# Kernel tuning notes

Measured on AMD Instinct MI355X. Metric: run time of the kernel, lower is better.

The kernel has to match this reference:

```python
import jax, jax.numpy as jnp
import numpy as np

G = 512       # field_size
SIGMA = 0.5   # causal kernel decay
H = 16        # num_heads


def _kernel_fft():
    # causal exponential kernel: k[i] = exp(-(center-i)/sigma) for i<=center else 0
    i = jnp.arange(G, dtype=jnp.float32)
    center = G // 2
    k = jnp.where(i <= center, jnp.exp(-(center - i) / SIGMA), 0.0)
    k = k / (k.sum() + 1e-8)
    return jnp.fft.rfft(k)  # [G//2+1] complex


def setup_inputs() -> dict:
    key = jax.random.key(0)
    ks = jax.random.split(key, 5)
    B, N, D = 4, 8192, 1024
    s = 1.0 / np.sqrt(D)
    return {
        "x": jax.random.normal(ks[0], (B, N, D), jnp.float32),
        "Wqkv": jax.random.normal(ks[1], (3 * D, D), jnp.float32) * s,
        "bqkv": jax.random.normal(ks[2], (3 * D,), jnp.float32) * 0.01,
        "Wout": jax.random.normal(ks[3], (D, D), jnp.float32) * s,
        "bout": jax.random.normal(ks[4], (D,), jnp.float32) * 0.01,
    }


def reference(x, Wqkv, bqkv, Wout, bout):
    B, N, D = x.shape
    hd = D // H
    qkv = x @ Wqkv.T + bqkv                       # [B,N,3D]
    q, k, v = jnp.split(qkv, 3, axis=-1)          # q is computed but unused (as in source)
    k = k.reshape(B, N, H, hd).transpose(0, 2, 1, 3)   # [B,H,N,hd]
    v = v.reshape(B, N, H, hd).transpose(0, 2, 1, 3)
    # map sequence positions to field bins
    seq_pos = jnp.arange(N, dtype=jnp.float32)
    field_idx = jnp.clip((seq_pos / max(N - 1, 1) * (G - 1)).astype(jnp.int32), 0, G - 1)  # [N]
    # deposit = v * |k|, scattered into the field buffer
    k_mag = jnp.linalg.norm(k, axis=-1, keepdims=True)  # [B,H,N,1]
    deposit = v * k_mag                                  # [B,H,N,hd]
    field = jnp.zeros((B, H, G, hd), x.dtype).at[:, :, field_idx, :].add(deposit)
    # causal (circular) convolution via FFT along field axis
    kf = _kernel_fft()
    field = jnp.fft.irfft(jnp.fft.rfft(field, axis=2) * kf[None, None, :, None], n=G, axis=2)
    # gather back at each token's bin
    out = field[:, :, field_idx, :]                      # [B,H,N,hd]
    out = out.transpose(0, 2, 1, 3).reshape(B, N, D)
    return out @ Wout.T + bout
```

## Files before the change

kernel.cpp:

```cpp
#include <hip/hip_runtime.h>

#define BB 4
#define NN 8192
#define DD 1024
#define HH 16
#define HD 64
#define GG 512

typedef short short8 __attribute__((ext_vector_type(8)));
typedef float f32x4 __attribute__((ext_vector_type(4)));

__device__ __forceinline__ unsigned short f2bf(float f) {
  union { float f; unsigned int u; } v; v.f = f;
  unsigned int r = v.u + 0x7FFFu + ((v.u >> 16) & 1u);
  return (unsigned short)(r >> 16);
}
__device__ __forceinline__ float bf2f(unsigned short b) {
  union { unsigned int u; float f; } v; v.u = ((unsigned int)b) << 16;
  return v.f;
}

__device__ __forceinline__ void gload16(const void* g, void* l) {
  __builtin_amdgcn_global_load_lds((const __attribute__((address_space(1))) void*)g,
                                   (__attribute__((address_space(3))) void*)l,
                                   16, 0, 0);
}

__global__ void cvt_all(const float* __restrict__ x, const float* __restrict__ Wqkv,
                        const float* __restrict__ Wout,
                        unsigned short* __restrict__ xb, unsigned short* __restrict__ wkb,
                        unsigned short* __restrict__ wvb, unsigned short* __restrict__ woutb) {
  const int total = 8388608 + 3 * 262144;
  int stride = gridDim.x * blockDim.x;
  for (int j = blockIdx.x * blockDim.x + threadIdx.x; j < total; j += stride) {
    const float4* s; ushort4* d; int r;
    if (j < 8388608) { s = (const float4*)x; d = (ushort4*)xb; r = j; }
    else {
      int q = j - 8388608; int seg = q >> 18; r = q & 262143;
      if (seg == 0)      { s = (const float4*)(Wqkv + 1048576); d = (ushort4*)wkb; }
      else if (seg == 1) { s = (const float4*)(Wqkv + 2097152); d = (ushort4*)wvb; }
      else               { s = (const float4*)Wout;             d = (ushort4*)woutb; }
    }
    float4 f = s[r];
    ushort4 u;
    u.x = f2bf(f.x); u.y = f2bf(f.y); u.z = f2bf(f.z); u.w = f2bf(f.w);
    d[r] = u;
  }
}

__global__ __launch_bounds__(256) void xw_kernel(
    const unsigned short* __restrict__ xb, const float* __restrict__ kw,
    unsigned short* __restrict__ xwb, float* __restrict__ sw) {
  __shared__ float w_l[20][16];
  __shared__ int mflag[20];
  const int bg = blockIdx.x;
  const int b = bg >> 9, g = bg & 511;
  const int t = threadIdx.x;
  int lo = (g * (NN - 1)) / (GG - 1) - 2;
  if (lo < 0) lo = 0;
  if (t < 20) {
    int n = lo + t;
    mflag[t] = (n < NN) && ((int)(((float)n / 8191.0f) * 511.0f) == g);
  }
  for (int u = t; u < 320; u += 256) {
    int ln = u >> 4, h = u & 15;
    int n = lo + ln;
    float w = 0.0f;
    if (n < NN && (int)(((float)n / 8191.0f) * 511.0f) == g)
      w = kw[((size_t)(b * NN + n)) * 16 + h];
    w_l[ln][h] = w;
  }
  __syncthreads();
  if (t < 16) {
    float s = 0.0f;
    #pragma unroll
    for (int ln = 0; ln < 20; ++ln) s += w_l[ln][t];
    sw[bg * 16 + t] = s;
  }
  float acc[16][4] = {};
  const int c0 = t * 4;
  for (int ln = 0; ln < 20; ++ln) {
    if (!mflag[ln]) continue;
    int n = lo + ln;
    ushort4 xv = *(const ushort4*)(xb + ((size_t)(b * NN + n)) * 1024 + c0);
    float x0 = bf2f(xv.x), x1 = bf2f(xv.y), x2 = bf2f(xv.z), x3 = bf2f(xv.w);
    #pragma unroll
    for (int h = 0; h < 16; ++h) {
      float w = w_l[ln][h];
      acc[h][0] += w * x0; acc[h][1] += w * x1;
      acc[h][2] += w * x2; acc[h][3] += w * x3;
    }
  }
  #pragma unroll
  for (int h = 0; h < 16; ++h) {
    ushort4 o;
    o.x = f2bf(acc[h][0]); o.y = f2bf(acc[h][1]);
    o.z = f2bf(acc[h][2]); o.w = f2bf(acc[h][3]);
    *(ushort4*)(xwb + ((size_t)h * 2048 + bg) * 1024 + c0) = o;
  }
}

__global__ __launch_bounds__(256, 2) void field_gemm(
    const unsigned short* __restrict__ xwb, const unsigned short* __restrict__ wvb,
    const float* __restrict__ sw, const float* __restrict__ bv,
    float* __restrict__ field2) {
  __shared__ __align__(16) unsigned short As[2][64 * 32];
  __shared__ __align__(16) unsigned short Bs[2][64 * 32];
  const int h = blockIdx.x >> 5;
  const int mb = blockIdx.x & 31;
  const int t = threadIdx.x;
  const int wv_ = t >> 6, lane = t & 63;
  const int l15 = lane & 15, sr = lane >> 4;

  const unsigned short* Ah = xwb + (size_t)h * 2048 * 1024 + (size_t)mb * 64 * 1024;
  const unsigned short* Bh = wvb + (size_t)h * 64 * 1024;

  const int srow = wv_ * 16 + (lane >> 2);
  const int sg = (lane & 3) ^ ((srow >> 1) & 3);
  const int dL = wv_ * 1024;

  const unsigned short* aG = Ah + (size_t)srow * 1024 + sg * 8;
  const unsigned short* bG = Bh + (size_t)srow * 1024 + sg * 8;

  auto stage = [&](int tt, int q) {
    gload16(aG + tt * 32, (char*)As[q] + dL);
    gload16(bG + tt * 32, (char*)Bs[q] + dL);
  };

  int aOff, bOff[4];
  {
    int r = wv_ * 16 + l15;
    aOff = r * 64 + ((sr ^ ((r >> 1) & 3)) * 16);
  }
  #pragma unroll
  for (int j = 0; j < 4; ++j) {
    int r = j * 16 + l15;
    bOff[j] = r * 64 + ((sr ^ ((r >> 1) & 3)) * 16);
  }

  f32x4 acc[4] = {};
  stage(0, 0);
  for (int tt = 0; tt < 32; ++tt) {
    if (tt + 1 < 32) {
      stage(tt + 1, (tt + 1) & 1);
      asm volatile("s_waitcnt vmcnt(2)" ::: "memory");
    } else {
      asm volatile("s_waitcnt vmcnt(0)" ::: "memory");
    }
    __builtin_amdgcn_s_barrier();
    const char* a = (const char*)As[tt & 1];
    const char* bb = (const char*)Bs[tt & 1];
    short8 aF = *(const short8*)(a + aOff);
    short8 bF[4];
    #pragma unroll
    for (int j = 0; j < 4; ++j) bF[j] = *(const short8*)(bb + bOff[j]);
    #pragma unroll
    for (int j = 0; j < 4; ++j)
      acc[j] = __builtin_amdgcn_mfma_f32_16x16x32_bf16(aF, bF[j], acc[j], 0, 0, 0);
    __builtin_amdgcn_s_barrier();
  }

  const int row0 = mb * 64 + wv_ * 16 + sr * 4;
  #pragma unroll
  for (int r = 0; r < 4; ++r) {
    float swv = sw[(row0 + r) * 16 + h];
    #pragma unroll
    for (int j = 0; j < 4; ++j) {
      int col = h * 64 + j * 16 + l15;
      field2[(size_t)(row0 + r) * 1024 + col] = acc[j][r] + swv * bv[col];
    }
  }
}

__global__ __launch_bounds__(256, 4) void gemm64(
    const unsigned short* __restrict__ A, const unsigned short* __restrict__ Bm,
    const float* __restrict__ bias, float* __restrict__ C,
    int M, int N, int K) {
  __shared__ __align__(16) unsigned short As[2][64 * 32];
  __shared__ __align__(16) unsigned short Bs[2][64 * 32];
  const int nb = N >> 6;
  const int mb = blockIdx.x / nb, nk = blockIdx.x % nb;
  const int t = threadIdx.x;
  const int wv_ = t >> 6, lane = t & 63;
  const int l15 = lane & 15, sr = lane >> 4;
  const int nt = K >> 5;

  const unsigned short* Ab = A + (size_t)mb * 64 * K;
  const unsigned short* Bb = Bm + (size_t)nk * 64 * K;

  const int srow = wv_ * 16 + (lane >> 2);
  const int sg = (lane & 3) ^ ((srow >> 1) & 3);
  const int dL = wv_ * 1024;

  const unsigned short* aG = Ab + (size_t)srow * K + sg * 8;
  const unsigned short* bG = Bb + (size_t)srow * K + sg * 8;

  auto stage = [&](int tt, int q) {
    gload16(aG + tt * 32, (char*)As[q] + dL);
    gload16(bG + tt * 32, (char*)Bs[q] + dL);
  };

  int aOff, bOff[4];
  {
    int r = wv_ * 16 + l15;
    aOff = r * 64 + ((sr ^ ((r >> 1) & 3)) * 16);
  }
  #pragma unroll
  for (int j = 0; j < 4; ++j) {
    int r = j * 16 + l15;
    bOff[j] = r * 64 + ((sr ^ ((r >> 1) & 3)) * 16);
  }

  f32x4 acc[4] = {};
  stage(0, 0);
  for (int tt = 0; tt < nt; ++tt) {
    if (tt + 1 < nt) {
      stage(tt + 1, (tt + 1) & 1);
      asm volatile("s_waitcnt vmcnt(2)" ::: "memory");
    } else {
      asm volatile("s_waitcnt vmcnt(0)" ::: "memory");
    }
    __builtin_amdgcn_s_barrier();
    const char* a = (const char*)As[tt & 1];
    const char* bb = (const char*)Bs[tt & 1];
    short8 aF = *(const short8*)(a + aOff);
    short8 bF[4];
    #pragma unroll
    for (int j = 0; j < 4; ++j) bF[j] = *(const short8*)(bb + bOff[j]);
    #pragma unroll
    for (int j = 0; j < 4; ++j)
      acc[j] = __builtin_amdgcn_mfma_f32_16x16x32_bf16(aF, bF[j], acc[j], 0, 0, 0);
    __builtin_amdgcn_s_barrier();
  }

  const int row0 = mb * 64 + wv_ * 16 + sr * 4;
  #pragma unroll
  for (int r = 0; r < 4; ++r) {
    #pragma unroll
    for (int j = 0; j < 4; ++j) {
      int col = nk * 64 + j * 16 + l15;
      C[(size_t)(row0 + r) * N + col] = acc[j][r] + bias[col];
    }
  }
}

__global__ void conv_kernel(const float* __restrict__ field2,
                            unsigned short* __restrict__ fconv2) {
  int i = blockIdx.x * blockDim.x + threadIdx.x;
  int c4 = i & 255;
  int bg = i >> 8;
  int b = bg >> 9, g = bg & 511;
  const float4* f4 = (const float4*)field2;
  float w = 0.86466471f;
  const float dec = 0.13533528f;
  float4 s = {0.f, 0.f, 0.f, 0.f};
  #pragma unroll
  for (int m = 0; m <= 20; ++m) {
    float4 v = f4[(size_t)((b << 9) + ((g + 256 + m) & 511)) * 256 + c4];
    s.x += w * v.x; s.y += w * v.y; s.z += w * v.z; s.w += w * v.w;
    w *= dec;
  }
  ushort4 o;
  o.x = f2bf(s.x); o.y = f2bf(s.y); o.z = f2bf(s.z); o.w = f2bf(s.w);
  *(ushort4*)(fconv2 + (size_t)bg * 1024 + c4 * 4) = o;
}

__global__ void expand_kernel(const float* __restrict__ small,
                              float* __restrict__ out) {
  const int total = 32768 * 256;
  int stride = gridDim.x * blockDim.x;
  for (int i = blockIdx.x * blockDim.x + threadIdx.x; i < total; i += stride) {
    int m = i >> 8;
    int b = m >> 13, n = m & (NN - 1);
    int g = (int)(((float)n / 8191.0f) * 511.0f);
    ((float4*)out)[i] = ((const float4*)small)[(((b << 9) + g) << 8) + (i & 255)];
  }
}

__global__ __launch_bounds__(512, 2) void gemm_knorm(
    const unsigned short* __restrict__ A, const unsigned short* __restrict__ Bm,
    const float* __restrict__ bias, float* __restrict__ Cout,
    int M, int N, int K) {
  __shared__ __align__(16) unsigned short smem[4 * 16384];

  const int t512 = threadIdx.x;
  const int wv = t512 >> 6, lane = t512 & 63;
  const int wm = wv >> 2, wn = wv & 3;
  const int l15 = lane & 15, sr = lane >> 4;
  const int nt = K >> 5;

  const int nwg = gridDim.x;
  const int lin = blockIdx.x;
  const int swz = (lin & 7) * (nwg >> 3) + (lin >> 3);
  const int gx = N >> 8;
  const int bm = (swz / gx) * 256;
  const int bn = (swz % gx) * 256;

  const int srow0 = wv * 16 + (lane >> 2);
  const int sg = (lane & 3) ^ ((srow0 >> 1) & 3);
  const int aL0 = wv * 1024;
  const int aL1 = 8192 + wv * 1024;

  const unsigned short* aG0 = A + (size_t)(bm + srow0) * K + sg * 8;
  const unsigned short* aG1 = A + (size_t)(bm + srow0 + 128) * K + sg * 8;
  const unsigned short* bG0 = Bm + (size_t)(bn + srow0) * K + sg * 8;
  const unsigned short* bG1 = Bm + (size_t)(bn + srow0 + 128) * K + sg * 8;

  auto stageA = [&](int t, int q) {
    char* base = (char*)smem + q * 32768;
    gload16(aG0 + (size_t)t * 32, base + aL0);
    gload16(aG1 + (size_t)t * 32, base + aL1);
  };
  auto stageB = [&](int t, int q) {
    char* base = (char*)smem + q * 32768;
    gload16(bG0 + (size_t)t * 32, base + 16384 + aL0);
    gload16(bG1 + (size_t)t * 32, base + 16384 + aL1);
  };

  int aOffB[8], bOffB[4];
  #pragma unroll
  for (int i = 0; i < 8; ++i) {
    int r = wm * 128 + i * 16 + l15;
    aOffB[i] = r * 64 + ((sr ^ ((r >> 1) & 3)) * 16);
  }
  #pragma unroll
  for (int j = 0; j < 4; ++j) {
    int r = wn * 64 + j * 16 + l15;
    bOffB[j] = r * 64 + ((sr ^ ((r >> 1) & 3)) * 16);
  }

  f32x4 acc[8][4] = {};

  stageA(0, 0); stageB(0, 0);
  stageA(1, 1); stageB(1, 1);
  stageA(2, 2); stageB(2, 2);
  asm volatile("s_waitcnt vmcnt(8)" ::: "memory");
  __builtin_amdgcn_s_barrier();

  for (int t = 0; t < nt; ++t) {
    const char* base = (const char*)smem + (t & 3) * 32768;
    short8 aF[8], bF[4];

    if (t + 3 < nt) stageA(t + 3, (t + 3) & 3);
    #pragma unroll
    for (int i = 0; i < 4; ++i) aF[i] = *(const short8*)(base + aOffB[i]);
    #pragma unroll
    for (int j = 0; j < 4; ++j) bF[j] = *(const short8*)(base + 16384 + bOffB[j]);
    __builtin_amdgcn_s_barrier();
    __builtin_amdgcn_s_setprio(1);
    #pragma unroll
    for (int i = 0; i < 4; ++i)
      #pragma unroll
      for (int j = 0; j < 4; ++j)
        acc[i][j] = __builtin_amdgcn_mfma_f32_16x16x32_bf16(aF[i], bF[j], acc[i][j], 0, 0, 0);
    __builtin_amdgcn_s_setprio(0);
    __builtin_amdgcn_s_barrier();

    if (t + 3 < nt) stageB(t + 3, (t + 3) & 3);
    #pragma unroll
    for (int i = 4; i < 8; ++i) aF[i] = *(const short8*)(base + aOffB[i]);
    {
      int rem = nt - 1 - t;
      if (rem >= 3)      asm volatile("s_waitcnt vmcnt(8)" ::: "memory");
      else if (rem == 2) asm volatile("s_waitcnt vmcnt(4)" ::: "memory");
      else               asm volatile("s_waitcnt vmcnt(0)" ::: "memory");
    }
    __builtin_amdgcn_s_barrier();
    __builtin_amdgcn_s_setprio(1);
    #pragma unroll
    for (int i = 4; i < 8; ++i)
      #pragma unroll
      for (int j = 0; j < 4; ++j)
        acc[i][j] = __builtin_amdgcn_mfma_f32_16x16x32_bf16(aF[i], bF[j], acc[i][j], 0, 0, 0);
    __builtin_amdgcn_s_setprio(0);
    __builtin_amdgcn_s_barrier();
  }

  const int hcol = (bn >> 6) + wn;
  float kb[4];
  #pragma unroll
  for (int j = 0; j < 4; ++j) kb[j] = bias[bn + wn * 64 + j * 16 + l15];
  #pragma unroll
  for (int i = 0; i < 8; ++i) {
    #pragma unroll
    for (int r = 0; r < 4; ++r) {
      float s = 0.0f;
      #pragma unroll
      for (int j = 0; j < 4; ++j) {
        float val = acc[i][j][r] + kb[j];
        s += val * val;
      }
      s += __shfl_xor(s, 1, 64);
      s += __shfl_xor(s, 2, 64);
      s += __shfl_xor(s, 4, 64);
      s += __shfl_xor(s, 8, 64);
      if (l15 == 0) {
        int row = bm + wm * 128 + i * 16 + sr * 4 + r;
        Cout[(size_t)row * 16 + hcol] = sqrtf(s);
      }
    }
  }
}

extern "C" void kernel_launch(void* const* d_in, const int* in_sizes, int n_in,
                              void* d_out, int out_size, void* d_ws, size_t ws_size,
                              hipStream_t stream) {
  const float* x    = (const float*)d_in[0];
  const float* Wqkv = (const float*)d_in[1];
  const float* bqkv = (const float*)d_in[2];
  const float* Wout = (const float*)d_in[3];
  const float* bout = (const float*)d_in[4];
  float* out = (float*)d_out;

  const size_t M = (size_t)BB * NN;

  char* ws = (char*)d_ws;
  size_t off = 0;
  unsigned short* xb    = (unsigned short*)(ws + off); off += M * DD * 2;
  unsigned short* wkb   = (unsigned short*)(ws + off); off += (size_t)DD * DD * 2;
  unsigned short* wvb   = (unsigned short*)(ws + off); off += (size_t)DD * DD * 2;
  unsigned short* woutb = (unsigned short*)(ws + off); off += (size_t)DD * DD * 2;
  float*          kw    = (float*)(ws + off);          off += M * HH * 4;
  unsigned short* xwb   = (unsigned short*)(ws + off); off += (size_t)HH*BB*GG*DD*2;
  float*          field2= (float*)(ws + off);          off += (size_t)BB*GG*DD*4;
  unsigned short* fconv2= (unsigned short*)(ws + off); off += (size_t)BB*GG*DD*2;
  float*          sw    = (float*)(ws + off);          off += (size_t)BB*GG*HH*4;
  float* small = (float*)xb;

  cvt_all<<<8960, 256, 0, stream>>>(x, Wqkv, Wout, xb, wkb, wvb, woutb);

  gemm_knorm<<<(DD / 256) * (M / 256), 512, 0, stream>>>(
      xb, wkb, bqkv + DD, kw, (int)M, DD, DD);

  xw_kernel<<<BB * GG, 256, 0, stream>>>(xb, kw, xwb, sw);

  field_gemm<<<HH * 32, 256, 0, stream>>>(xwb, wvb, sw, bqkv + 2 * DD, field2);

  conv_kernel<<<BB * GG, 256, 0, stream>>>(field2, fconv2);

  gemm64<<<(BB * GG / 64) * (DD / 64), 256, 0, stream>>>(
      fconv2, woutb, bout, small, BB * GG, DD, DD);

  expand_kernel<<<4096, 256, 0, stream>>>(small, out);
}
```

Measured before the change: 229.1 us.

## Compute key-norm GEMM in FP8 using scaled MFMA with bias folded into K

Replaces the bf16 key projection GEMM used only for per-head key norms with an FP8 GEMM built on the 16x16x128 scaled MFMA. The bias is folded in as an extra K column (x gets a column of ones), and the weights are pre-scaled by 32 to keep them in FP8 range. A new conversion kernel produces padded 1152-byte FP8 rows from the bf16 x copy. The aim is fewer MFMA instructions and half the operand bytes, paid for with an extra conversion pass over x and lower precision in the key norms.

```diff
diff --git a/kernel.cpp b/kernel.cpp
--- a/kernel.cpp
+++ b/kernel.cpp
@@ -9,6 +9,8 @@
 
 typedef short short8 __attribute__((ext_vector_type(8)));
 typedef float f32x4 __attribute__((ext_vector_type(4)));
+typedef int int4v __attribute__((ext_vector_type(4)));
+typedef int int8v __attribute__((ext_vector_type(8)));
 
 __device__ __forceinline__ unsigned short f2bf(float f) {
   union { float f; unsigned int u; } v; v.f = f;
@@ -28,23 +30,159 @@
 
 __global__ void cvt_all(const float* __restrict__ x, const float* __restrict__ Wqkv,
                         const float* __restrict__ Wout,
-                        unsigned short* __restrict__ xb, unsigned short* __restrict__ wkb,
+                        unsigned short* __restrict__ xb,
                         unsigned short* __restrict__ wvb, unsigned short* __restrict__ woutb) {
-  const int total = 8388608 + 3 * 262144;
+  const int total = 8388608 + 2 * 262144;
   int stride = gridDim.x * blockDim.x;
   for (int j = blockIdx.x * blockDim.x + threadIdx.x; j < total; j += stride) {
     const float4* s; ushort4* d; int r;
     if (j < 8388608) { s = (const float4*)x; d = (ushort4*)xb; r = j; }
     else {
       int q = j - 8388608; int seg = q >> 18; r = q & 262143;
-      if (seg == 0)      { s = (const float4*)(Wqkv + 1048576); d = (ushort4*)wkb; }
-      else if (seg == 1) { s = (const float4*)(Wqkv + 2097152); d = (ushort4*)wvb; }
-      else               { s = (const float4*)Wout;             d = (ushort4*)woutb; }
+      if (seg == 0) { s = (const float4*)(Wqkv + 2097152); d = (ushort4*)wvb; }
+      else          { s = (const float4*)Wout;             d = (ushort4*)woutb; }
     }
     float4 f = s[r];
     ushort4 u;
     u.x = f2bf(f.x); u.y = f2bf(f.y); u.z = f2bf(f.z); u.w = f2bf(f.w);
     d[r] = u;
+  }
+}
+
+__global__ __launch_bounds__(256) void cvt8_kernel(
+    const unsigned short* __restrict__ xb, const float* __restrict__ Wqkv,
+    const float* __restrict__ bqkv,
+    unsigned char* __restrict__ xb8, unsigned char* __restrict__ wk8) {
+  int r = blockIdx.x;
+  bool isX = r < 32768;
+  unsigned char* dst = isX ? xb8 + (size_t)r * 1152
+                           : wk8 + (size_t)(r - 32768) * 1152;
+  for (int c = threadIdx.x; c < 288; c += 256) {
+    unsigned int word = 0;
+    if (c < 256) {
+      float f0, f1, f2, f3;
+      if (isX) {
+        ushort4 v = *(const ushort4*)(xb + (size_t)r * 1024 + c * 4);
+        f0 = bf2f(v.x); f1 = bf2f(v.y); f2 = bf2f(v.z); f3 = bf2f(v.w);
+      } else {
+        const float* wr = Wqkv + 1048576 + (size_t)(r - 32768) * 1024 + c * 4;
+        f0 = wr[0] * 32.0f; f1 = wr[1] * 32.0f; f2 = wr[2] * 32.0f; f3 = wr[3] * 32.0f;
+      }
+      word = __builtin_amdgcn_cvt_pk_fp8_f32(f0, f1, word, false);
+      word = __builtin_amdgcn_cvt_pk_fp8_f32(f2, f3, word, true);
+    } else if (c == 256) {
+      float f0 = isX ? 1.0f : 32.0f * bqkv[1024 + (r - 32768)];
+      word = __builtin_amdgcn_cvt_pk_fp8_f32(f0, 0.0f, 0, false);
+    }
+    *(unsigned int*)(dst + c * 4) = word;
+  }
+}
+
+__global__ __launch_bounds__(512, 2) void gemm_knorm8(
+    const unsigned char* __restrict__ A,
+    const unsigned char* __restrict__ Bm,
+    float* __restrict__ Cout, int M) {
+  __shared__ __align__(16) unsigned char smem[2][2][32768];
+
+  const int t512 = threadIdx.x;
+  const int wv = t512 >> 6, lane = t512 & 63;
+  const int wm = wv >> 2, wn = wv & 3;
+  const int l15 = lane & 15, sr = lane >> 4;
+
+  const int nwg = gridDim.x;
+  const int lin = blockIdx.x;
+  const int swz = (lin & 7) * (nwg >> 3) + (lin >> 3);
+  const int bm = (swz >> 2) * 256;
+  const int bn = (swz & 3) * 256;
+
+  const int rrl = lane >> 3;
+  const int ps  = lane & 7;
+
+  auto stage = [&](int t, int q) {
+    #pragma unroll
+    for (int it = 0; it < 4; ++it) {
+      int ra = wv * 32 + it * 8 + rrl;
+      int gs = ps ^ (ra & 7);
+      gload16(A + (size_t)(bm + ra) * 1152 + t * 128 + gs * 16,
+              &smem[q][0][(wv * 32 + it * 8) * 128]);
+      gload16(Bm + (size_t)(bn + ra) * 1152 + t * 128 + gs * 16,
+              &smem[q][1][(wv * 32 + it * 8) * 128]);
+    }
+  };
+
+  int aOff[8][2], bOff[4][2];
+  #pragma unroll
+  for (int i = 0; i < 8; ++i) {
+    int r = wm * 128 + i * 16 + l15;
+    #pragma unroll
+    for (int h = 0; h < 2; ++h)
+      aOff[i][h] = r * 128 + (((sr * 2 + h) ^ (r & 7)) * 16);
+  }
+  #pragma unroll
+  for (int j = 0; j < 4; ++j) {
+    int r = wn * 64 + j * 16 + l15;
+    #pragma unroll
+    for (int h = 0; h < 2; ++h)
+      bOff[j][h] = r * 128 + (((sr * 2 + h) ^ (r & 7)) * 16);
+  }
+
+  f32x4 acc[8][4] = {};
+
+  stage(0, 0); stage(1, 1);
+
+  for (int t = 0; t < 9; ++t) {
+    if (t < 8) asm volatile("s_waitcnt vmcnt(8)" ::: "memory");
+    else       asm volatile("s_waitcnt vmcnt(0)" ::: "memory");
+    __builtin_amdgcn_s_barrier();
+
+    const unsigned char* ab = smem[t & 1][0];
+    const unsigned char* bb = smem[t & 1][1];
+    int8v b8[4];
+    #pragma unroll
+    for (int j = 0; j < 4; ++j) {
+      int4v lo = *(const int4v*)(bb + bOff[j][0]);
+      int4v hi = *(const int4v*)(bb + bOff[j][1]);
+      int8v v; v[0]=lo[0]; v[1]=lo[1]; v[2]=lo[2]; v[3]=lo[3];
+               v[4]=hi[0]; v[5]=hi[1]; v[6]=hi[2]; v[7]=hi[3];
+      b8[j] = v;
+    }
+    __builtin_amdgcn_s_setprio(1);
+    #pragma unroll
+    for (int i = 0; i < 8; ++i) {
+      int4v lo = *(const int4v*)(ab + aOff[i][0]);
+      int4v hi = *(const int4v*)(ab + aOff[i][1]);
+      int8v a8; a8[0]=lo[0]; a8[1]=lo[1]; a8[2]=lo[2]; a8[3]=lo[3];
+                a8[4]=hi[0]; a8[5]=hi[1]; a8[6]=hi[2]; a8[7]=hi[3];
+      #pragma unroll
+      for (int j = 0; j < 4; ++j)
+        acc[i][j] = __builtin_amdgcn_mfma_scale_f32_16x16x128_f8f6f4(
+            a8, b8[j], acc[i][j], 0, 0, 0, 127, 0, 127);
+    }
+    __builtin_amdgcn_s_setprio(0);
+    __builtin_amdgcn_s_barrier();
+    if (t + 2 < 9) stage(t + 2, t & 1);
+  }
+
+  const int hcol = (bn >> 6) + wn;
+  #pragma unroll
+  for (int i = 0; i < 8; ++i) {
+    #pragma unroll
+    for (int r = 0; r < 4; ++r) {
+      float s = 0.0f;
+      #pragma unroll
+      for (int j = 0; j < 4; ++j) {
+        float val = acc[i][j][r] * 0.03125f;
+        s += val * val;
+      }
+      s += __shfl_xor(s, 1, 64);
+      s += __shfl_xor(s, 2, 64);
+      s += __shfl_xor(s, 4, 64);
+      s += __shfl_xor(s, 8, 64);
+      if (l15 == 0) {
+        int row = bm + wm * 128 + i * 16 + sr * 4 + r;
+        Cout[(size_t)row * 16 + hcol] = sqrtf(s);
+      }
+    }
   }
 }
 
@@ -277,131 +415,6 @@
   }
 }
 
-__global__ __launch_bounds__(512, 2) void gemm_knorm(
-    const unsigned short* __restrict__ A, const unsigned short* __restrict__ Bm,
-    const float* __restrict__ bias, float* __restrict__ Cout,
-    int M, int N, int K) {
-  __shared__ __align__(16) unsigned short smem[4 * 16384];
-
-  const int t512 = threadIdx.x;
-  const int wv = t512 >> 6, lane = t512 & 63;
-  const int wm = wv >> 2, wn = wv & 3;
-  const int l15 = lane & 15, sr = lane >> 4;
-  const int nt = K >> 5;
-
-  const int nwg = gridDim.x;
-  const int lin = blockIdx.x;
-  const int swz = (lin & 7) * (nwg >> 3) + (lin >> 3);
-  const int gx = N >> 8;
-  const int bm = (swz / gx) * 256;
-  const int bn = (swz % gx) * 256;
-
-  const int srow0 = wv * 16 + (lane >> 2);
-  const int sg = (lane & 3) ^ ((srow0 >> 1) & 3);
-  const int aL0 = wv * 1024;
-  const int aL1 = 8192 + wv * 1024;
-
-  const unsigned short* aG0 = A + (size_t)(bm + srow0) * K + sg * 8;
-  const unsigned short* aG1 = A + (size_t)(bm + srow0 + 128) * K + sg * 8;
-  const unsigned short* bG0 = Bm + (size_t)(bn + srow0) * K + sg * 8;
-  const unsigned short* bG1 = Bm + (size_t)(bn + srow0 + 128) * K + sg * 8;
-
-  auto stageA = [&](int t, int q) {
-    char* base = (char*)smem + q * 32768;
-    gload16(aG0 + (size_t)t * 32, base + aL0);
-    gload16(aG1 + (size_t)t * 32, base + aL1);
-  };
-  auto stageB = [&](int t, int q) {
-    char* base = (char*)smem + q * 32768;
-    gload16(bG0 + (size_t)t * 32, base + 16384 + aL0);
-    gload16(bG1 + (size_t)t * 32, base + 16384 + aL1);
-  };
-
-  int aOffB[8], bOffB[4];
-  #pragma unroll
-  for (int i = 0; i < 8; ++i) {
-    int r = wm * 128 + i * 16 + l15;
-    aOffB[i] = r * 64 + ((sr ^ ((r >> 1) & 3)) * 16);
-  }
-  #pragma unroll
-  for (int j = 0; j < 4; ++j) {
-    int r = wn * 64 + j * 16 + l15;
-    bOffB[j] = r * 64 + ((sr ^ ((r >> 1) & 3)) * 16);
-  }
-
-  f32x4 acc[8][4] = {};
-
-  stageA(0, 0); stageB(0, 0);
-  stageA(1, 1); stageB(1, 1);
-  stageA(2, 2); stageB(2, 2);
-  asm volatile("s_waitcnt vmcnt(8)" ::: "memory");
-  __builtin_amdgcn_s_barrier();
-
-  for (int t = 0; t < nt; ++t) {
-    const char* base = (const char*)smem + (t & 3) * 32768;
-    short8 aF[8], bF[4];
-
-    if (t + 3 < nt) stageA(t + 3, (t + 3) & 3);
-    #pragma unroll
-    for (int i = 0; i < 4; ++i) aF[i] = *(const short8*)(base + aOffB[i]);
-    #pragma unroll
-    for (int j = 0; j < 4; ++j) bF[j] = *(const short8*)(base + 16384 + bOffB[j]);
-    __builtin_amdgcn_s_barrier();
-    __builtin_amdgcn_s_setprio(1);
-    #pragma unroll
-    for (int i = 0; i < 4; ++i)
-      #pragma unroll
-      for (int j = 0; j < 4; ++j)
-        acc[i][j] = __builtin_amdgcn_mfma_f32_16x16x32_bf16(aF[i], bF[j], acc[i][j], 0, 0, 0);
-    __builtin_amdgcn_s_setprio(0);
-    __builtin_amdgcn_s_barrier();
-
-    if (t + 3 < nt) stageB(t + 3, (t + 3) & 3);
-    #pragma unroll
-    for (int i = 4; i < 8; ++i) aF[i] = *(const short8*)(base + aOffB[i]);
-    {
-      int rem = nt - 1 - t;
-      if (rem >= 3)      asm volatile("s_waitcnt vmcnt(8)" ::: "memory");
-      else if (rem == 2) asm volatile("s_waitcnt vmcnt(4)" ::: "memory");
-      else               asm volatile("s_waitcnt vmcnt(0)" ::: "memory");
-    }
-    __builtin_amdgcn_s_barrier();
-    __builtin_amdgcn_s_setprio(1);
-    #pragma unroll
-    for (int i = 4; i < 8; ++i)
-      #pragma unroll
-      for (int j = 0; j < 4; ++j)
-        acc[i][j] = __builtin_amdgcn_mfma_f32_16x16x32_bf16(aF[i], bF[j], acc[i][j], 0, 0, 0);
-    __builtin_amdgcn_s_setprio(0);
-    __builtin_amdgcn_s_barrier();
-  }
-
-  const int hcol = (bn >> 6) + wn;
-  float kb[4];
-  #pragma unroll
-  for (int j = 0; j < 4; ++j) kb[j] = bias[bn + wn * 64 + j * 16 + l15];
-  #pragma unroll
-  for (int i = 0; i < 8; ++i) {
-    #pragma unroll
-    for (int r = 0; r < 4; ++r) {
-      float s = 0.0f;
-      #pragma unroll
-      for (int j = 0; j < 4; ++j) {
-        float val = acc[i][j][r] + kb[j];
-        s += val * val;
-      }
-      s += __shfl_xor(s, 1, 64);
-      s += __shfl_xor(s, 2, 64);
-      s += __shfl_xor(s, 4, 64);
-      s += __shfl_xor(s, 8, 64);
-      if (l15 == 0) {
-        int row = bm + wm * 128 + i * 16 + sr * 4 + r;
-        Cout[(size_t)row * 16 + hcol] = sqrtf(s);
-      }
-    }
-  }
-}
-
 extern "C" void kernel_launch(void* const* d_in, const int* in_sizes, int n_in,
                               void* d_out, int out_size, void* d_ws, size_t ws_size,
                               hipStream_t stream) {
@@ -417,7 +430,8 @@
   char* ws = (char*)d_ws;
   size_t off = 0;
   unsigned short* xb    = (unsigned short*)(ws + off); off += M * DD * 2;
-  unsigned short* wkb   = (unsigned short*)(ws + off); off += (size_t)DD * DD * 2;
+  unsigned char*  xb8   = (unsigned char*)(ws + off);  off += M * 1152;
+  unsigned char*  wk8   = (unsigned char*)(ws + off);  off += (size_t)DD * 1152;
   unsigned short* wvb   = (unsigned short*)(ws + off); off += (size_t)DD * DD * 2;
   unsigned short* woutb = (unsigned short*)(ws + off); off += (size_t)DD * DD * 2;
   float*          kw    = (float*)(ws + off);          off += M * HH * 4;
@@ -427,10 +441,10 @@
   float*          sw    = (float*)(ws + off);          off += (size_t)BB*GG*HH*4;
   float* small = (float*)xb;
 
-  cvt_all<<<8960, 256, 0, stream>>>(x, Wqkv, Wout, xb, wkb, wvb, woutb);
-
-  gemm_knorm<<<(DD / 256) * (M / 256), 512, 0, stream>>>(
-      xb, wkb, bqkv + DD, kw, (int)M, DD, DD);
+  cvt_all<<<8704, 256, 0, stream>>>(x, Wqkv, Wout, xb, wvb, woutb);
+  cvt8_kernel<<<(int)M + DD, 256, 0, stream>>>(xb, Wqkv, bqkv, xb8, wk8);
+
+  gemm_knorm8<<<4 * (M / 256), 512, 0, stream>>>(xb8, wk8, kw, (int)M);
 
   xw_kernel<<<BB * GG, 256, 0, stream>>>(xb, kw, xwb, sw);
 
```

Result: slower. 596.4 us (+160.3%).
